# Kernel tuning notes

Measured on AMD Instinct MI355X. Metric: run time of the kernel, lower is better.

## Reference

```python
import jax, jax.numpy as jnp
import numpy as np

BLOCK_LEN = 64  # chunk length l


def setup_inputs() -> dict:
    key = jax.random.key(0)
    k1, k2, k3 = jax.random.split(key, 3)
    b, s, h, p, n = 8, 4096, 16, 64, 64
    X = jax.random.normal(k1, (b, s, h, p), jnp.float32)
    # A must be negative for numerically stable decays (exp(cumsum diffs) <= 1),
    # matching real Mamba2 where A_log parameterizes a negative decay rate.
    A = -0.1 * jnp.abs(jax.random.normal(k2, (b, s, h), jnp.float32))
    B = jax.random.normal(k3, (b, s, h, n), jnp.float32)
    return {"X": X, "A": A, "B": B}


def reference(X, A, B):
    L = BLOCK_LEN
    b, s, h, p = X.shape
    n = B.shape[-1]
    c = s // L  # number of chunks

    # b (c l) ... -> b c l ...
    Xb = X.reshape(b, c, L, h, p)
    Bb = B.reshape(b, c, L, h, n)
    Ab = jnp.transpose(A.reshape(b, c, L, h), (0, 3, 1, 2))  # (b, h, c, l)

    A_cumsum = jnp.cumsum(Ab, axis=-1)  # (b, h, c, l)

    # Fused decay-einsum: states[b,c,h,p,n] =
    #   sum_l B[b,c,l,h,n] * exp(A_cumsum[b,h,c,-1] - A_cumsum[b,h,c,l]) * X[b,c,l,h,p]
    decay_states = jnp.exp(A_cumsum[..., -1:] - A_cumsum)  # (b, h, c, l)
    states = jnp.einsum('bclhn,bhcl,bclhp->bchpn', Bb, decay_states, Xb)

    # Prepend zero initial states along chunk dim -> (b, c+1, h, p, n)
    states = jnp.concatenate([jnp.zeros_like(states[:, :1]), states], axis=1)

    # Inter-chunk recurrence via exp(segsum(padded chunk totals)).
    padded_A = jnp.pad(A_cumsum[..., -1], ((0, 0), (0, 0), (1, 0)))  # (b, h, c+1)
    cs = jnp.cumsum(padded_A, axis=-1)
    Z = c + 1
    diff = cs[..., :, None] - cs[..., None, :]  # (b, h, Z, Z), row - col
    mask = jnp.tril(jnp.ones((Z, Z), dtype=bool))  # row >= col
    decay_chunk = jnp.where(mask, jnp.exp(diff), 0.0)  # (b, h, Z, Z)

    new_states = jnp.einsum('bhzc,bchpn->bzhpn', decay_chunk, states)
    return new_states[:, -1]  # (b, h, p, n)
```

## Files before the change

### kernel.cpp

```cpp
#include <hip/hip_runtime.h>
#include <hip/hip_bf16.h>


constexpr int Bn = 8;
constexpr int S  = 4096;
constexpr int H  = 16;
constexpr int P  = 64;
constexpr int N  = 64;

constexpr int NCH = 8;
constexpr int TCH = S / NCH;
constexpr int TB  = 8;

__global__ __launch_bounds__(256) void scan_weights(
    const float* __restrict__ A, float* __restrict__ W) {
  const int pair = blockIdx.x;
  const int bb = pair / H, hh = pair % H;
  const int tid = threadIdx.x;
  constexpr int TPT = S / 256;

  float vals[TPT];
  float local = 0.f;
  const int t0 = tid * TPT;
  #pragma unroll
  for (int i = 0; i < TPT; ++i) {
    float a = A[((size_t)bb * S + t0 + i) * H + hh];
    local += a;
    vals[i] = local;
  }

  __shared__ float sums[256];
  sums[tid] = local;
  __syncthreads();
  for (int off = 1; off < 256; off <<= 1) {
    float v = sums[tid];
    float add = (tid >= off) ? sums[tid - off] : 0.f;
    __syncthreads();
    sums[tid] = v + add;
    __syncthreads();
  }
  const float total = sums[255];
  const float excl  = sums[tid] - local;

  float* Wp = W + (size_t)pair * S;
  #pragma unroll
  for (int i = 0; i < TPT; ++i) {
    Wp[t0 + i] = __expf(total - (excl + vals[i]));
  }
}

__global__ __launch_bounds__(256) void outer_accum(
    const float* __restrict__ X, const float* __restrict__ Bm,
    const float* __restrict__ W, float* __restrict__ out) {
  __shared__ float Xs[TB][P];
  __shared__ float Bs[TB][N];

  const int bid  = blockIdx.x;
  const int pair = bid / NCH;
  const int ch   = bid % NCH;
  const int tid  = threadIdx.x;
  const int t_begin = ch * TCH;

  const int n0 = (tid & 15) * 4;
  const int p0 = (tid >> 4) * 4;

  const int lrow = (tid & 127) >> 4;
  const int lcol = (tid & 15) * 4;
  const bool isB = tid >= 128;

  const int bb = pair / H, hh = pair % H;
  const size_t baseX = ((size_t)bb * S * H + hh) * (size_t)P;
  const size_t baseB = ((size_t)bb * S * H + hh) * (size_t)N;
  const float* Wp = W + (size_t)pair * S;

  float acc[4][4];
  #pragma unroll
  for (int i = 0; i < 4; ++i)
    #pragma unroll
    for (int j = 0; j < 4; ++j) acc[i][j] = 0.f;

  for (int t0 = t_begin; t0 < t_begin + TCH; t0 += TB) {
    const int t = t0 + lrow;
    if (!isB) {
      const float w = Wp[t];
      const float4 v = *(const float4*)(X + baseX + (size_t)t * H * P + lcol);
      float4 sv; sv.x = v.x * w; sv.y = v.y * w; sv.z = v.z * w; sv.w = v.w * w;
      *(float4*)&Xs[lrow][lcol] = sv;
    } else {
      *(float4*)&Bs[lrow][lcol] = *(const float4*)(Bm + baseB + (size_t)t * H * N + lcol);
    }
    __syncthreads();

    #pragma unroll
    for (int tt = 0; tt < TB; ++tt) {
      const float4 xv = *(const float4*)&Xs[tt][p0];
      const float4 bv = *(const float4*)&Bs[tt][n0];
      const float xs[4] = {xv.x, xv.y, xv.z, xv.w};
      const float bs[4] = {bv.x, bv.y, bv.z, bv.w};
      #pragma unroll
      for (int i = 0; i < 4; ++i)
        #pragma unroll
        for (int j = 0; j < 4; ++j)
          acc[i][j] = fmaf(xs[i], bs[j], acc[i][j]);
    }
    __syncthreads();
  }

  float* outp = out + (size_t)pair * P * N;
  #pragma unroll
  for (int i = 0; i < 4; ++i)
    #pragma unroll
    for (int j = 0; j < 4; ++j)
      atomicAdd(&outp[(size_t)(p0 + i) * N + (n0 + j)], acc[i][j]);
}

extern "C" void kernel_launch(void* const* d_in, const int* in_sizes, int n_in,
                              void* d_out, int out_size, void* d_ws, size_t ws_size,
                              hipStream_t stream) {
  const float* X = (const float*)d_in[0];
  const float* A = (const float*)d_in[1];
  const float* B = (const float*)d_in[2];
  float* out = (float*)d_out;
  float* W   = (float*)d_ws;

  hipMemsetAsync(d_out, 0, (size_t)out_size * sizeof(float), stream);

  scan_weights<<<Bn * H, 256, 0, stream>>>(A, W);
  outer_accum<<<Bn * H * NCH, 256, 0, stream>>>(X, B, W, out);
}
```

Measured before the change: 324.5 us.

## Rewrite as segment-scan pipeline with register-tiled outer products and split reduction

```diff
diff --git a/kernel.cpp b/kernel.cpp
--- a/kernel.cpp
+++ b/kernel.cpp
@@ -1,117 +1,141 @@
 #include <hip/hip_runtime.h>
-#include <hip/hip_bf16.h>
+#include <math.h>
 
 
 constexpr int Bn = 8;
 constexpr int S  = 4096;
 constexpr int H  = 16;
-constexpr int P  = 64;
-constexpr int N  = 64;
+constexpr int Pp = 64;
+constexpr int Nn = 64;
+constexpr int SEG  = 128;
+constexpr int NSEG = S / SEG;
 
-constexpr int NCH = 8;
-constexpr int TCH = S / NCH;
-constexpr int TB  = 8;
-
-__global__ __launch_bounds__(256) void scan_weights(
-    const float* __restrict__ A, float* __restrict__ W) {
-  const int pair = blockIdx.x;
-  const int bb = pair / H, hh = pair % H;
+__global__ __launch_bounds__(256) void seg_sums(const float* __restrict__ A,
+                                                float* __restrict__ ss) {
+  const int bb  = blockIdx.x >> 5;
+  const int seg = blockIdx.x & 31;
+  __shared__ float lds[SEG * H];
+  const float* src = A + ((size_t)bb * S + (size_t)seg * SEG) * H;
   const int tid = threadIdx.x;
-  constexpr int TPT = S / 256;
-
-  float vals[TPT];
-  float local = 0.f;
-  const int t0 = tid * TPT;
   #pragma unroll
-  for (int i = 0; i < TPT; ++i) {
-    float a = A[((size_t)bb * S + t0 + i) * H + hh];
-    local += a;
-    vals[i] = local;
-  }
-
-  __shared__ float sums[256];
-  sums[tid] = local;
+  for (int i = 0; i < 2; ++i)
+    ((float4*)lds)[tid + i * 256] = ((const float4*)src)[tid + i * 256];
   __syncthreads();
-  for (int off = 1; off < 256; off <<= 1) {
-    float v = sums[tid];
-    float add = (tid >= off) ? sums[tid - off] : 0.f;
-    __syncthreads();
-    sums[tid] = v + add;
-    __syncthreads();
-  }
-  const float total = sums[255];
-  const float excl  = sums[tid] - local;
-
-  float* Wp = W + (size_t)pair * S;
-  #pragma unroll
-  for (int i = 0; i < TPT; ++i) {
-    Wp[t0 + i] = __expf(total - (excl + vals[i]));
+  if (tid < H) {
+    float s = 0.f;
+    for (int t = 0; t < SEG; ++t) s += lds[t * H + tid];
+    ss[((size_t)bb * NSEG + seg) * H + tid] = s;
   }
 }
 
-__global__ __launch_bounds__(256) void outer_accum(
-    const float* __restrict__ X, const float* __restrict__ Bm,
-    const float* __restrict__ W, float* __restrict__ out) {
-  __shared__ float Xs[TB][P];
-  __shared__ float Bs[TB][N];
+__global__ __launch_bounds__(256) void seg_scan(const float* __restrict__ ss,
+                                                float* __restrict__ pfx,
+                                                float* __restrict__ tot) {
+  const int pid = threadIdx.x;
+  if (pid >= Bn * H) return;
+  const int bb = pid >> 4, h = pid & 15;
+  float run = 0.f;
+  for (int s = 0; s < NSEG; ++s) {
+    pfx[(size_t)pid * NSEG + s] = run;
+    run += ss[((size_t)bb * NSEG + s) * H + h];
+  }
+  tot[pid] = run;
+}
 
-  const int bid  = blockIdx.x;
-  const int pair = bid / NCH;
-  const int ch   = bid % NCH;
-  const int tid  = threadIdx.x;
-  const int t_begin = ch * TCH;
+__global__ __launch_bounds__(256) void outer_k(const float* __restrict__ X,
+                                               const float* __restrict__ Bm,
+                                               const float* __restrict__ A,
+                                               const float* __restrict__ pfx,
+                                               const float* __restrict__ tot,
+                                               float* __restrict__ part, int SC) {
+  const int blk  = blockIdx.x;
+  const int pair = blk / SC, sc = blk % SC;
+  const int bb = pair >> 4, hh = pair & 15;
+  const int tid = threadIdx.x, w = tid >> 6, lane = tid & 63;
+  const int TPW = S / (SC * 4);
+  const int t0  = sc * (S / SC) + w * TPW;
+  const int r = lane >> 3, c = lane & 7;
 
-  const int n0 = (tid & 15) * 4;
-  const int p0 = (tid >> 4) * 4;
+  float acc[8][8];
+  #pragma unroll
+  for (int i = 0; i < 8; ++i)
+    #pragma unroll
+    for (int j = 0; j < 8; ++j) acc[i][j] = 0.f;
 
-  const int lrow = (tid & 127) >> 4;
-  const int lcol = (tid & 15) * 4;
-  const bool isB = tid >= 128;
+  float run = pfx[(size_t)pair * NSEG + t0 / SEG];
+  const float total = tot[pair];
 
-  const int bb = pair / H, hh = pair % H;
-  const size_t baseX = ((size_t)bb * S * H + hh) * (size_t)P;
-  const size_t baseB = ((size_t)bb * S * H + hh) * (size_t)N;
-  const float* Wp = W + (size_t)pair * S;
+  const float* Arow = A + ((size_t)bb * S + t0) * H + hh;
+  const float* Xrow = X + (((size_t)bb * S + t0) * H + hh) * Pp + r * 8;
+  const float* Brow = Bm + (((size_t)bb * S + t0) * H + hh) * Nn + c * 8;
+  constexpr size_t TS = (size_t)H * Pp;
 
-  float acc[4][4];
-  #pragma unroll
-  for (int i = 0; i < 4; ++i)
+  #pragma unroll 2
+  for (int t = 0; t < TPW; ++t) {
+    const float a = Arow[(size_t)t * H];
+    run += a;
+    const float wgt = __expf(total - run);
+    const float4 x0 = *(const float4*)(Xrow + (size_t)t * TS);
+    const float4 x1 = *(const float4*)(Xrow + (size_t)t * TS + 4);
+    const float4 b0 = *(const float4*)(Brow + (size_t)t * TS);
+    const float4 b1 = *(const float4*)(Brow + (size_t)t * TS + 4);
+    const float xs[8] = {x0.x * wgt, x0.y * wgt, x0.z * wgt, x0.w * wgt,
+                         x1.x * wgt, x1.y * wgt, x1.z * wgt, x1.w * wgt};
+    const float bs[8] = {b0.x, b0.y, b0.z, b0.w, b1.x, b1.y, b1.z, b1.w};
     #pragma unroll
-    for (int j = 0; j < 4; ++j) acc[i][j] = 0.f;
-
-  for (int t0 = t_begin; t0 < t_begin + TCH; t0 += TB) {
-    const int t = t0 + lrow;
-    if (!isB) {
-      const float w = Wp[t];
-      const float4 v = *(const float4*)(X + baseX + (size_t)t * H * P + lcol);
-      float4 sv; sv.x = v.x * w; sv.y = v.y * w; sv.z = v.z * w; sv.w = v.w * w;
-      *(float4*)&Xs[lrow][lcol] = sv;
-    } else {
-      *(float4*)&Bs[lrow][lcol] = *(const float4*)(Bm + baseB + (size_t)t * H * N + lcol);
-    }
-    __syncthreads();
-
-    #pragma unroll
-    for (int tt = 0; tt < TB; ++tt) {
-      const float4 xv = *(const float4*)&Xs[tt][p0];
-      const float4 bv = *(const float4*)&Bs[tt][n0];
-      const float xs[4] = {xv.x, xv.y, xv.z, xv.w};
-      const float bs[4] = {bv.x, bv.y, bv.z, bv.w};
+    for (int i = 0; i < 8; ++i)
       #pragma unroll
-      for (int i = 0; i < 4; ++i)
-        #pragma unroll
-        for (int j = 0; j < 4; ++j)
-          acc[i][j] = fmaf(xs[i], bs[j], acc[i][j]);
-    }
-    __syncthreads();
+      for (int j = 0; j < 8; ++j)
+        acc[i][j] = fmaf(xs[i], bs[j], acc[i][j]);
   }
 
-  float* outp = out + (size_t)pair * P * N;
-  #pragma unroll
-  for (int i = 0; i < 4; ++i)
+  __shared__ float red[2][4096];
+  if (w >= 2) {
     #pragma unroll
-    for (int j = 0; j < 4; ++j)
-      atomicAdd(&outp[(size_t)(p0 + i) * N + (n0 + j)], acc[i][j]);
+    for (int i = 0; i < 8; ++i)
+      #pragma unroll
+      for (int j = 0; j < 8; ++j) red[w - 2][(i * 8 + j) * 64 + lane] = acc[i][j];
+  }
+  __syncthreads();
+  if (w < 2) {
+    #pragma unroll
+    for (int i = 0; i < 8; ++i)
+      #pragma unroll
+      for (int j = 0; j < 8; ++j) acc[i][j] += red[w][(i * 8 + j) * 64 + lane];
+  }
+  __syncthreads();
+  if (w == 1) {
+    #pragma unroll
+    for (int i = 0; i < 8; ++i)
+      #pragma unroll
+      for (int j = 0; j < 8; ++j) red[0][(i * 8 + j) * 64 + lane] = acc[i][j];
+  }
+  __syncthreads();
+  if (w == 0) {
+    float* base = part + (size_t)blk * 4096;
+    #pragma unroll
+    for (int i = 0; i < 8; ++i) {
+      #pragma unroll
+      for (int j = 0; j < 8; ++j) acc[i][j] += red[0][(i * 8 + j) * 64 + lane];
+      *(float4*)(base + (r * 8 + i) * 64 + c * 8)     =
+          make_float4(acc[i][0], acc[i][1], acc[i][2], acc[i][3]);
+      *(float4*)(base + (r * 8 + i) * 64 + c * 8 + 4) =
+          make_float4(acc[i][4], acc[i][5], acc[i][6], acc[i][7]);
+    }
+  }
+}
+
+__global__ __launch_bounds__(256) void reduce_k(const float* __restrict__ part,
+                                                float* __restrict__ out, int SC) {
+  const int idx  = blockIdx.x * 256 + threadIdx.x;
+  const int pair = idx >> 10;
+  const int off  = (idx & 1023) * 4;
+  float4 s = make_float4(0.f, 0.f, 0.f, 0.f);
+  for (int sc = 0; sc < SC; ++sc) {
+    const float4 v = *(const float4*)(part + ((size_t)(pair * SC + sc)) * 4096 + off);
+    s.x += v.x; s.y += v.y; s.z += v.z; s.w += v.w;
+  }
+  *(float4*)(out + (size_t)pair * 4096 + off) = s;
 }
 
 extern "C" void kernel_launch(void* const* d_in, const int* in_sizes, int n_in,
@@ -121,10 +145,18 @@
   const float* A = (const float*)d_in[1];
   const float* B = (const float*)d_in[2];
   float* out = (float*)d_out;
-  float* W   = (float*)d_ws;
 
-  hipMemsetAsync(d_out, 0, (size_t)out_size * sizeof(float), stream);
+  int SC = 8;
+  const size_t misc = (size_t)(Bn * NSEG * H + Bn * H * NSEG + Bn * H) * sizeof(float);
+  while (SC > 1 && (size_t)Bn * H * SC * 4096 * sizeof(float) + misc > ws_size) SC >>= 1;
 
-  scan_weights<<<Bn * H, 256, 0, stream>>>(A, W);
-  outer_accum<<<Bn * H * NCH, 256, 0, stream>>>(X, B, W, out);
+  float* part = (float*)d_ws;
+  float* ss   = part + (size_t)Bn * H * SC * 4096;
+  float* pfx  = ss + (size_t)Bn * NSEG * H;
+  float* tot  = pfx + (size_t)Bn * H * NSEG;
+
+  seg_sums<<<Bn * NSEG, 256, 0, stream>>>(A, ss);
+  seg_scan<<<1, 256, 0, stream>>>(ss, pfx, tot);
+  outer_k<<<Bn * H * SC, 256, 0, stream>>>(X, B, A, pfx, tot, part, SC);
+  reduce_k<<<(Bn * H * Pp * Nn) / 4 / 256, 256, 0, stream>>>(part, out, SC);
 }
```

Measured after the change: 341.9 us. 1.05x slower.
